# Performance work log

Measured on AMD Instinct MI355X. Metric: run time of the kernel, lower is better.

Reference implementation:

```python
import jax, jax.numpy as jnp
import numpy as np

BATCH, B_BANDS, C, T = 32, 5, 64, 128
D_EMBED, D_S = 64, 16


def setup_inputs() -> dict:
    key = jax.random.key(0)
    ks = jax.random.split(key, 8)
    x = jax.random.normal(ks[0], (BATCH, B_BANDS, C, T), dtype=jnp.float32)
    # sparse binary physical adjacency with self-loops (avoid all-masked rows)
    adj = (jax.random.uniform(ks[1], (C, C)) < 0.3).astype(jnp.float32)
    adj = adj.at[jnp.arange(C), jnp.arange(C)].set(1.0)
    active_mask = jnp.ones((BATCH, T, B_BANDS), dtype=jnp.float32)
    alpha = jax.random.uniform(ks[2], (BATCH, T, B_BANDS), dtype=jnp.float32) + 0.1
    active_alpha = alpha / alpha.sum(axis=-1, keepdims=True)
    # per-band Linear(1, d_embed): weight (d_embed,1) flattened to (d_embed,), bias (d_embed,)
    W_e = jax.random.normal(ks[3], (B_BANDS, D_EMBED), dtype=jnp.float32)  # kaiming-ish for fan_in=1
    b_e = jax.random.uniform(ks[4], (B_BANDS, D_EMBED), dtype=jnp.float32) * 2.0 - 1.0
    Wq = jax.random.normal(ks[5], (D_S, D_EMBED), dtype=jnp.float32) / np.sqrt(D_EMBED)
    Wk = jax.random.normal(ks[6], (D_S, D_EMBED), dtype=jnp.float32) / np.sqrt(D_EMBED)
    return {"x": x, "adj": adj, "active_mask": active_mask, "active_alpha": active_alpha,
            "W_e": W_e, "b_e": b_e, "Wq": Wq, "Wk": Wk}


def reference(x, adj, active_mask, active_alpha, W_e, b_e, Wq, Wk):
    # x: (batch, B, C, T) -> x_t: (batch, T, B, C)
    x_t = jnp.transpose(x, (0, 3, 1, 2))
    d_s = Wq.shape[0]
    # per-band Linear(1, d_embed), all bands vectorized: e (batch, T, B, C, d_embed)
    e = x_t[..., None] * W_e[None, None, :, None, :] + b_e[None, None, :, None, :]
    q = jnp.einsum('btncd,sd->btncs', e, Wq)
    k = jnp.einsum('btncd,sd->btncs', e, Wk)
    # scores per band: (batch, T, B, C, C)
    s = jnp.einsum('btnis,btnjs->btnij', q, k) / jnp.sqrt(jnp.asarray(d_s, x.dtype))
    neg_inf = jnp.finfo(s.dtype).min
    s = jnp.where(adj[None, None, None, :, :] > 0, s, neg_inf)
    P = jax.nn.softmax(s, axis=-1)  # row-stochastic on adj neighborhoods
    w = active_alpha * active_mask  # (batch, T, B)
    P_func = jnp.einsum('btn,btnij->btij', w, P)  # (batch, T, C, C)
    e_mean = e.mean(axis=3)  # (batch, T, B, d_embed) mean over electrodes
    embed_accum = jnp.einsum('btn,btnd->btd', active_mask, e_mean)
    active_count = jnp.clip(active_mask.sum(axis=-1, keepdims=True), 1.0, None)
    embeddings_mean = embed_accum / active_count
    return P_func, embeddings_mean
```

## Files before the change

kernel.cpp:

```cpp
#include <hip/hip_runtime.h>
#include <math.h>

#define NBANDS 5
#define T_TILE 4
#define PFUNC_ELEMS (32*128*64*64)
#define LOG2E 1.4426950408889634f

#define DPP_ADD(x, ctrl) \
    ((x) + __int_as_float(__builtin_amdgcn_update_dpp(0, __float_as_int(x), (ctrl), 0xF, 0xF, true)))

__global__ __launch_bounds__(512) void bfp_kernel(
        const float* __restrict__ x,
        const float* __restrict__ adj,
        const float* __restrict__ amask,
        const float* __restrict__ alpha,
        const float* __restrict__ We,
        const float* __restrict__ be,
        const float* __restrict__ Wq,
        const float* __restrict__ Wk,
        float* __restrict__ out) {
    const int bid = blockIdx.x;
    const int blk = (bid & 7) * 128 + (bid >> 3);
    const int bt0 = blk * T_TILE;
    const int b = bt0 >> 7;
    const int t0 = bt0 & 127;
    const int tid = threadIdx.x;

    __shared__ __align__(16) float x_s[T_TILE][NBANDS][64];
    __shared__ float xbar_s[T_TILE][NBANDS], xmax_s[T_TILE][NBANDS], xmin_s[T_TILE][NBANDS];
    __shared__ float w_s[T_TILE][NBANDS], mask_s[T_TILE][NBANDS];
    __shared__ float acw_s[NBANDS], bcw_s[NBANDS];

    const int i = tid >> 3;
    const int j0 = (tid & 7) << 3;

    const float4 a0 = *(const float4*)(adj + i * 64 + j0);
    const float4 a1 = *(const float4*)(adj + i * 64 + j0 + 4);

    float4 xstage;
    if (tid < NBANDS * 64)
        xstage = *(const float4*)(x + ((size_t)b * 320 + tid) * 128 + t0);

    if (tid >= 512 - T_TILE * NBANDS) {
        const int idx = tid - (512 - T_TILE * NBANDS);
        const size_t base = ((size_t)b * 128 + t0) * NBANDS;
        const int t = idx / NBANDS, n = idx % NBANDS;
        float mk = amask[base + idx];
        mask_s[t][n] = mk;
        w_s[t][n] = alpha[base + idx] * mk;
    }

    {
        const int wvid = tid >> 6;
        const int lane = tid & 63;
        if (wvid < NBANDS) {
            const int n = wvid;
            const int s = lane >> 2;
            const int d0c = (lane & 3) * 16;
            float u = 0.f, v = 0.f, w = 0.f;
            #pragma unroll
            for (int dd = 0; dd < 16; ++dd) {
                int d = d0c + dd;
                float we = We[n * 64 + d], bb = be[n * 64 + d];
                float wq = Wq[s * 64 + d], wk = Wk[s * 64 + d];
                u = fmaf(wq, we, u);
                v = fmaf(wk, we, v);
                w = fmaf(wq, bb, w);
            }
            #pragma unroll
            for (int mk = 1; mk <= 2; mk <<= 1) {
                u += __shfl_xor(u, mk);
                v += __shfl_xor(v, mk);
                w += __shfl_xor(w, mk);
            }
            float ac = u * v, bc = w * v;
            #pragma unroll
            for (int mk = 4; mk <= 32; mk <<= 1) {
                ac += __shfl_xor(ac, mk);
                bc += __shfl_xor(bc, mk);
            }
            if (lane == 0) {
                acw_s[n] = 0.25f * LOG2E * ac;
                bcw_s[n] = 0.25f * LOG2E * bc;
            }
        }
    }

    if (tid < NBANDS * 64) {
        const int n = tid >> 6, c = tid & 63;
        x_s[0][n][c] = xstage.x;
        x_s[1][n][c] = xstage.y;
        x_s[2][n][c] = xstage.z;
        x_s[3][n][c] = xstage.w;
    }
    __syncthreads();

    {
        const int wv = tid >> 6, lane = tid & 63;
        for (int pair = wv; pair < T_TILE * NBANDS; pair += 8) {
            const int t = pair & 3, n = pair >> 2;
            float v = x_s[t][n][lane];
            float sm = v, mx = v, mn = v;
            #pragma unroll
            for (int mk = 32; mk >= 1; mk >>= 1) {
                sm += __shfl_xor(sm, mk);
                mx = fmaxf(mx, __shfl_xor(mx, mk));
                mn = fminf(mn, __shfl_xor(mn, mk));
            }
            if (lane == 0) {
                xbar_s[t][n] = sm * (1.f / 64.f);
                xmax_s[t][n] = mx;
                xmin_s[t][n] = mn;
            }
        }
    }
    __syncthreads();

    if (tid < T_TILE * 64) {
        const int t = tid >> 6, d = tid & 63;
        float cnt = 0.f, accm = 0.f;
        #pragma unroll
        for (int n = 0; n < NBANDS; ++n) {
            cnt += mask_s[t][n];
            accm += mask_s[t][n] * fmaf(xbar_s[t][n], We[n * 64 + d], be[n * 64 + d]);
        }
        out[PFUNC_ELEMS + (size_t)(bt0 + t) * 64 + d] = accm / fmaxf(cnt, 1.f);
    }

    for (int t = 0; t < T_TILE; ++t) {
        float4 xv0[NBANDS], xv1[NBANDS];
        float gi[NBANDS];
        #pragma unroll
        for (int n = 0; n < NBANDS; ++n) {
            xv0[n] = ((const float4*)(&x_s[t][n][j0]))[0];
            xv1[n] = ((const float4*)(&x_s[t][n][j0]))[1];
            gi[n]  = x_s[t][n][i];
        }

        float acc[8];
        #pragma unroll
        for (int jj = 0; jj < 8; ++jj) acc[jj] = 0.f;

        #pragma unroll
        for (int n = 0; n < NBANDS; ++n) {
            const float g2 = fmaf(acw_s[n], gi[n], bcw_s[n]);
            const float negm = -fmaxf(g2 * xmax_s[t][n], g2 * xmin_s[t][n]);
            float e0 = __builtin_amdgcn_exp2f(fmaf(g2, xv0[n].x, negm));
            float e1 = __builtin_amdgcn_exp2f(fmaf(g2, xv0[n].y, negm));
            float e2 = __builtin_amdgcn_exp2f(fmaf(g2, xv0[n].z, negm));
            float e3 = __builtin_amdgcn_exp2f(fmaf(g2, xv0[n].w, negm));
            float e4 = __builtin_amdgcn_exp2f(fmaf(g2, xv1[n].x, negm));
            float e5 = __builtin_amdgcn_exp2f(fmaf(g2, xv1[n].y, negm));
            float e6 = __builtin_amdgcn_exp2f(fmaf(g2, xv1[n].z, negm));
            float e7 = __builtin_amdgcn_exp2f(fmaf(g2, xv1[n].w, negm));
            float z0 = e0 * a0.x;
            z0 = fmaf(e1, a0.y, z0);
            z0 = fmaf(e2, a0.z, z0);
            z0 = fmaf(e3, a0.w, z0);
            float z1 = e4 * a1.x;
            z1 = fmaf(e5, a1.y, z1);
            z1 = fmaf(e6, a1.z, z1);
            z1 = fmaf(e7, a1.w, z1);
            float Z = z0 + z1;
            Z = DPP_ADD(Z, 0xB1);
            Z = DPP_ADD(Z, 0x4E);
            Z = DPP_ADD(Z, 0x141);
            const float sc = w_s[t][n] * __builtin_amdgcn_rcpf(fmaxf(Z, 1e-30f));
            acc[0] = fmaf(e0, sc, acc[0]);
            acc[1] = fmaf(e1, sc, acc[1]);
            acc[2] = fmaf(e2, sc, acc[2]);
            acc[3] = fmaf(e3, sc, acc[3]);
            acc[4] = fmaf(e4, sc, acc[4]);
            acc[5] = fmaf(e5, sc, acc[5]);
            acc[6] = fmaf(e6, sc, acc[6]);
            acc[7] = fmaf(e7, sc, acc[7]);
        }

        float4* outp = (float4*)(out + ((size_t)(bt0 + t) * 64 + i) * 64 + j0);
        outp[0] = make_float4(acc[0] * a0.x, acc[1] * a0.y, acc[2] * a0.z, acc[3] * a0.w);
        outp[1] = make_float4(acc[4] * a1.x, acc[5] * a1.y, acc[6] * a1.z, acc[7] * a1.w);
    }
}

extern "C" void kernel_launch(void* const* d_in, const int* in_sizes, int n_in,
                              void* d_out, int out_size, void* d_ws, size_t ws_size,
                              hipStream_t stream) {
    const float* x     = (const float*)d_in[0];
    const float* adj   = (const float*)d_in[1];
    const float* amask = (const float*)d_in[2];
    const float* alpha = (const float*)d_in[3];
    const float* We    = (const float*)d_in[4];
    const float* be    = (const float*)d_in[5];
    const float* Wq    = (const float*)d_in[6];
    const float* Wk    = (const float*)d_in[7];
    float* out = (float*)d_out;

    bfp_kernel<<<1024, 512, 0, stream>>>(x, adj, amask, alpha, We, be, Wq, Wk, out);
}
```

Baseline: 30.95 us.

## Split into prep kernel for transpose/stats and per-timestep main kernel

Adds a prep kernel that transposes x into a workspace (b,t,n,c) layout and precomputes per-(b,t,n) max/min/mean, masked alpha and the band coefficients once. The main kernel then processes one timestep per block (4096 blocks) and reads these precomputed values instead of redoing reductions and coefficient dot products in every block. This removes redundant per-block setup and syncs, and gives more, smaller blocks. The cost is a second launch and an extra round trip through global memory for x. The old fused kernel stays as a fallback for when the workspace is too small.

```diff
diff --git a/kernel.cpp b/kernel.cpp
--- a/kernel.cpp
+++ b/kernel.cpp
@@ -2,82 +2,217 @@
 #include <math.h>
 
 #define NBANDS 5
-#define T_TILE 4
 #define PFUNC_ELEMS (32*128*64*64)
 #define LOG2E 1.4426950408889634f
 
+#define WS_XT    0
+#define WS_STATS 1310720
+#define WS_MASK  1392640
+#define WS_COEF  1413120
+#define WS_FLOATS_NEEDED 1413136ull
+
 #define DPP_ADD(x, ctrl) \
     ((x) + __int_as_float(__builtin_amdgcn_update_dpp(0, __float_as_int(x), (ctrl), 0xF, 0xF, true)))
 
-__global__ __launch_bounds__(512) void bfp_kernel(
+__global__ __launch_bounds__(256) void bfp_prep_kernel(
         const float* __restrict__ x,
-        const float* __restrict__ adj,
         const float* __restrict__ amask,
         const float* __restrict__ alpha,
-        const float* __restrict__ We,
-        const float* __restrict__ be,
-        const float* __restrict__ Wq,
-        const float* __restrict__ Wk,
+        const float* __restrict__ We, const float* __restrict__ be,
+        const float* __restrict__ Wq, const float* __restrict__ Wk,
+        float* __restrict__ ws) {
+    const int bid = blockIdx.x;
+    const int b = bid / NBANDS, n = bid % NBANDS;
+    const int tid = threadIdx.x;
+    __shared__ float xt[64][129];
+
+    for (int idx = tid; idx < 64 * 32; idx += 256) {
+        const int c = idx >> 5, q = idx & 31;
+        float4 v = *(const float4*)(x + (((size_t)b * NBANDS + n) * 64 + c) * 128 + q * 4);
+        xt[c][q * 4 + 0] = v.x;
+        xt[c][q * 4 + 1] = v.y;
+        xt[c][q * 4 + 2] = v.z;
+        xt[c][q * 4 + 3] = v.w;
+    }
+    __syncthreads();
+
+    for (int idx = tid; idx < 128 * 16; idx += 256) {
+        const int t = idx >> 4, cq = idx & 15;
+        float4 v = make_float4(xt[cq * 4 + 0][t], xt[cq * 4 + 1][t],
+                               xt[cq * 4 + 2][t], xt[cq * 4 + 3][t]);
+        *(float4*)(ws + WS_XT + (((size_t)b * 128 + t) * NBANDS + n) * 64 + cq * 4) = v;
+    }
+
+    if (tid < 128) {
+        const int t = tid;
+        float mx = xt[0][t], mn = mx, sm = mx;
+        #pragma unroll 8
+        for (int c = 1; c < 64; ++c) {
+            float v = xt[c][t];
+            mx = fmaxf(mx, v);
+            mn = fminf(mn, v);
+            sm += v;
+        }
+        const size_t sidx = ((size_t)b * 128 + t) * NBANDS + n;
+        const float am = amask[sidx];
+        ((float4*)(ws + WS_STATS))[sidx] =
+            make_float4(mx, mn, alpha[sidx] * am, sm * (1.f / 64.f));
+        ws[WS_MASK + sidx] = am;
+    }
+
+    if (b == 0 && tid < 16) {
+        const int s = tid;
+        float u = 0.f, v = 0.f, w = 0.f;
+        for (int d = 0; d < 64; ++d) {
+            const float we = We[n * 64 + d], bb = be[n * 64 + d];
+            u = fmaf(Wq[s * 64 + d], we, u);
+            v = fmaf(Wk[s * 64 + d], we, v);
+            w = fmaf(Wq[s * 64 + d], bb, w);
+        }
+        float ac = u * v, bc = w * v;
+        #pragma unroll
+        for (int mk = 1; mk <= 8; mk <<= 1) {
+            ac += __shfl_xor(ac, mk);
+            bc += __shfl_xor(bc, mk);
+        }
+        if (s == 0) {
+            ws[WS_COEF + n]     = 0.25f * LOG2E * ac;
+            ws[WS_COEF + 8 + n] = 0.25f * LOG2E * bc;
+        }
+    }
+}
+
+__global__ __launch_bounds__(512) void bfp_main_kernel(
+        const float* __restrict__ adj,
+        const float* __restrict__ We, const float* __restrict__ be,
+        const float* __restrict__ ws,
+        float* __restrict__ out) {
+    const int bid = blockIdx.x;
+    const int bt = (bid & 7) * 512 + (bid >> 3);
+    const int tid = threadIdx.x;
+    const int i = tid >> 3;
+    const int j0 = (tid & 7) << 3;
+
+    const float* xtp = ws + WS_XT + (size_t)bt * 320;
+    const float4* stp = (const float4*)(ws + WS_STATS) + (size_t)bt * NBANDS;
+
+    const float4 a0 = *(const float4*)(adj + i * 64 + j0);
+    const float4 a1 = *(const float4*)(adj + i * 64 + j0 + 4);
+
+    if (tid < 64) {
+        float cnt = 0.f, accm = 0.f;
+        #pragma unroll
+        for (int n = 0; n < NBANDS; ++n) {
+            const float mk = ws[WS_MASK + (size_t)bt * NBANDS + n];
+            cnt += mk;
+            accm += mk * fmaf(stp[n].w, We[n * 64 + tid], be[n * 64 + tid]);
+        }
+        out[PFUNC_ELEMS + (size_t)bt * 64 + tid] = accm / fmaxf(cnt, 1.f);
+    }
+
+    float acc[8];
+    #pragma unroll
+    for (int jj = 0; jj < 8; ++jj) acc[jj] = 0.f;
+
+    #pragma unroll
+    for (int n = 0; n < NBANDS; ++n) {
+        const float4 st = stp[n];
+        const float gi = xtp[n * 64 + i];
+        const float4 xv0 = *(const float4*)(xtp + n * 64 + j0);
+        const float4 xv1 = *(const float4*)(xtp + n * 64 + j0 + 4);
+        const float g2 = fmaf(ws[WS_COEF + n], gi, ws[WS_COEF + 8 + n]);
+        const float negm = -fmaxf(g2 * st.x, g2 * st.y);
+        float e0 = __builtin_amdgcn_exp2f(fmaf(g2, xv0.x, negm));
+        float e1 = __builtin_amdgcn_exp2f(fmaf(g2, xv0.y, negm));
+        float e2 = __builtin_amdgcn_exp2f(fmaf(g2, xv0.z, negm));
+        float e3 = __builtin_amdgcn_exp2f(fmaf(g2, xv0.w, negm));
+        float e4 = __builtin_amdgcn_exp2f(fmaf(g2, xv1.x, negm));
+        float e5 = __builtin_amdgcn_exp2f(fmaf(g2, xv1.y, negm));
+        float e6 = __builtin_amdgcn_exp2f(fmaf(g2, xv1.z, negm));
+        float e7 = __builtin_amdgcn_exp2f(fmaf(g2, xv1.w, negm));
+        float z0 = e0 * a0.x;
+        z0 = fmaf(e1, a0.y, z0);
+        z0 = fmaf(e2, a0.z, z0);
+        z0 = fmaf(e3, a0.w, z0);
+        float z1 = e4 * a1.x;
+        z1 = fmaf(e5, a1.y, z1);
+        z1 = fmaf(e6, a1.z, z1);
+        z1 = fmaf(e7, a1.w, z1);
+        float Z = z0 + z1;
+        Z = DPP_ADD(Z, 0xB1);
+        Z = DPP_ADD(Z, 0x4E);
+        Z = DPP_ADD(Z, 0x141);
+        const float sc = st.z * __builtin_amdgcn_rcpf(fmaxf(Z, 1e-30f));
+        acc[0] = fmaf(e0, sc, acc[0]);
+        acc[1] = fmaf(e1, sc, acc[1]);
+        acc[2] = fmaf(e2, sc, acc[2]);
+        acc[3] = fmaf(e3, sc, acc[3]);
+        acc[4] = fmaf(e4, sc, acc[4]);
+        acc[5] = fmaf(e5, sc, acc[5]);
+        acc[6] = fmaf(e6, sc, acc[6]);
+        acc[7] = fmaf(e7, sc, acc[7]);
+    }
+
+    float4* outp = (float4*)(out + ((size_t)bt * 64 + i) * 64 + j0);
+    outp[0] = make_float4(acc[0] * a0.x, acc[1] * a0.y, acc[2] * a0.z, acc[3] * a0.w);
+    outp[1] = make_float4(acc[4] * a1.x, acc[5] * a1.y, acc[6] * a1.z, acc[7] * a1.w);
+}
+
+__global__ __launch_bounds__(512) void bfp_fallback_kernel(
+        const float* __restrict__ x, const float* __restrict__ adj,
+        const float* __restrict__ amask, const float* __restrict__ alpha,
+        const float* __restrict__ We, const float* __restrict__ be,
+        const float* __restrict__ Wq, const float* __restrict__ Wk,
         float* __restrict__ out) {
     const int bid = blockIdx.x;
     const int blk = (bid & 7) * 128 + (bid >> 3);
-    const int bt0 = blk * T_TILE;
+    const int bt0 = blk * 4;
     const int b = bt0 >> 7;
     const int t0 = bt0 & 127;
     const int tid = threadIdx.x;
 
-    __shared__ __align__(16) float x_s[T_TILE][NBANDS][64];
-    __shared__ float xbar_s[T_TILE][NBANDS], xmax_s[T_TILE][NBANDS], xmin_s[T_TILE][NBANDS];
-    __shared__ float w_s[T_TILE][NBANDS], mask_s[T_TILE][NBANDS];
+    __shared__ __align__(16) float x_s[4][NBANDS][64];
+    __shared__ float xbar_s[4][NBANDS], xmax_s[4][NBANDS], xmin_s[4][NBANDS];
+    __shared__ float w_s[4][NBANDS], mask_s[4][NBANDS];
     __shared__ float acw_s[NBANDS], bcw_s[NBANDS];
 
     const int i = tid >> 3;
     const int j0 = (tid & 7) << 3;
-
     const float4 a0 = *(const float4*)(adj + i * 64 + j0);
     const float4 a1 = *(const float4*)(adj + i * 64 + j0 + 4);
 
     float4 xstage;
     if (tid < NBANDS * 64)
         xstage = *(const float4*)(x + ((size_t)b * 320 + tid) * 128 + t0);
-
-    if (tid >= 512 - T_TILE * NBANDS) {
-        const int idx = tid - (512 - T_TILE * NBANDS);
+    if (tid >= 512 - 4 * NBANDS) {
+        const int idx = tid - (512 - 4 * NBANDS);
         const size_t base = ((size_t)b * 128 + t0) * NBANDS;
         const int t = idx / NBANDS, n = idx % NBANDS;
         float mk = amask[base + idx];
         mask_s[t][n] = mk;
         w_s[t][n] = alpha[base + idx] * mk;
     }
-
     {
-        const int wvid = tid >> 6;
-        const int lane = tid & 63;
+        const int wvid = tid >> 6, lane = tid & 63;
         if (wvid < NBANDS) {
-            const int n = wvid;
-            const int s = lane >> 2;
-            const int d0c = (lane & 3) * 16;
+            const int n = wvid, s = lane >> 2, d0c = (lane & 3) * 16;
             float u = 0.f, v = 0.f, w = 0.f;
             #pragma unroll
             for (int dd = 0; dd < 16; ++dd) {
                 int d = d0c + dd;
                 float we = We[n * 64 + d], bb = be[n * 64 + d];
-                float wq = Wq[s * 64 + d], wk = Wk[s * 64 + d];
-                u = fmaf(wq, we, u);
-                v = fmaf(wk, we, v);
-                w = fmaf(wq, bb, w);
+                u = fmaf(Wq[s * 64 + d], we, u);
+                v = fmaf(Wk[s * 64 + d], we, v);
+                w = fmaf(Wq[s * 64 + d], bb, w);
             }
             #pragma unroll
             for (int mk = 1; mk <= 2; mk <<= 1) {
-                u += __shfl_xor(u, mk);
-                v += __shfl_xor(v, mk);
-                w += __shfl_xor(w, mk);
+                u += __shfl_xor(u, mk); v += __shfl_xor(v, mk); w += __shfl_xor(w, mk);
             }
             float ac = u * v, bc = w * v;
             #pragma unroll
             for (int mk = 4; mk <= 32; mk <<= 1) {
-                ac += __shfl_xor(ac, mk);
-                bc += __shfl_xor(bc, mk);
+                ac += __shfl_xor(ac, mk); bc += __shfl_xor(bc, mk);
             }
             if (lane == 0) {
                 acw_s[n] = 0.25f * LOG2E * ac;
@@ -85,19 +220,15 @@
             }
         }
     }
-
     if (tid < NBANDS * 64) {
         const int n = tid >> 6, c = tid & 63;
-        x_s[0][n][c] = xstage.x;
-        x_s[1][n][c] = xstage.y;
-        x_s[2][n][c] = xstage.z;
-        x_s[3][n][c] = xstage.w;
+        x_s[0][n][c] = xstage.x; x_s[1][n][c] = xstage.y;
+        x_s[2][n][c] = xstage.z; x_s[3][n][c] = xstage.w;
     }
     __syncthreads();
-
     {
         const int wv = tid >> 6, lane = tid & 63;
-        for (int pair = wv; pair < T_TILE * NBANDS; pair += 8) {
+        for (int pair = wv; pair < 4 * NBANDS; pair += 8) {
             const int t = pair & 3, n = pair >> 2;
             float v = x_s[t][n][lane];
             float sm = v, mx = v, mn = v;
@@ -109,14 +240,12 @@
             }
             if (lane == 0) {
                 xbar_s[t][n] = sm * (1.f / 64.f);
-                xmax_s[t][n] = mx;
-                xmin_s[t][n] = mn;
+                xmax_s[t][n] = mx; xmin_s[t][n] = mn;
             }
         }
     }
     __syncthreads();
-
-    if (tid < T_TILE * 64) {
+    if (tid < 4 * 64) {
         const int t = tid >> 6, d = tid & 63;
         float cnt = 0.f, accm = 0.f;
         #pragma unroll
@@ -126,21 +255,18 @@
         }
         out[PFUNC_ELEMS + (size_t)(bt0 + t) * 64 + d] = accm / fmaxf(cnt, 1.f);
     }
-
-    for (int t = 0; t < T_TILE; ++t) {
+    for (int t = 0; t < 4; ++t) {
         float4 xv0[NBANDS], xv1[NBANDS];
         float gi[NBANDS];
         #pragma unroll
         for (int n = 0; n < NBANDS; ++n) {
             xv0[n] = ((const float4*)(&x_s[t][n][j0]))[0];
             xv1[n] = ((const float4*)(&x_s[t][n][j0]))[1];
-            gi[n]  = x_s[t][n][i];
-        }
-
+            gi[n] = x_s[t][n][i];
+        }
         float acc[8];
         #pragma unroll
         for (int jj = 0; jj < 8; ++jj) acc[jj] = 0.f;
-
         #pragma unroll
         for (int n = 0; n < NBANDS; ++n) {
             const float g2 = fmaf(acw_s[n], gi[n], bcw_s[n]);
@@ -154,28 +280,17 @@
             float e6 = __builtin_amdgcn_exp2f(fmaf(g2, xv1[n].z, negm));
             float e7 = __builtin_amdgcn_exp2f(fmaf(g2, xv1[n].w, negm));
             float z0 = e0 * a0.x;
-            z0 = fmaf(e1, a0.y, z0);
-            z0 = fmaf(e2, a0.z, z0);
-            z0 = fmaf(e3, a0.w, z0);
+            z0 = fmaf(e1, a0.y, z0); z0 = fmaf(e2, a0.z, z0); z0 = fmaf(e3, a0.w, z0);
             float z1 = e4 * a1.x;
-            z1 = fmaf(e5, a1.y, z1);
-            z1 = fmaf(e6, a1.z, z1);
-            z1 = fmaf(e7, a1.w, z1);
+            z1 = fmaf(e5, a1.y, z1); z1 = fmaf(e6, a1.z, z1); z1 = fmaf(e7, a1.w, z1);
             float Z = z0 + z1;
-            Z = DPP_ADD(Z, 0xB1);
-            Z = DPP_ADD(Z, 0x4E);
-            Z = DPP_ADD(Z, 0x141);
+            Z = DPP_ADD(Z, 0xB1); Z = DPP_ADD(Z, 0x4E); Z = DPP_ADD(Z, 0x141);
             const float sc = w_s[t][n] * __builtin_amdgcn_rcpf(fmaxf(Z, 1e-30f));
-            acc[0] = fmaf(e0, sc, acc[0]);
-            acc[1] = fmaf(e1, sc, acc[1]);
-            acc[2] = fmaf(e2, sc, acc[2]);
-            acc[3] = fmaf(e3, sc, acc[3]);
-            acc[4] = fmaf(e4, sc, acc[4]);
-            acc[5] = fmaf(e5, sc, acc[5]);
-            acc[6] = fmaf(e6, sc, acc[6]);
-            acc[7] = fmaf(e7, sc, acc[7]);
-        }
-
+            acc[0] = fmaf(e0, sc, acc[0]); acc[1] = fmaf(e1, sc, acc[1]);
+            acc[2] = fmaf(e2, sc, acc[2]); acc[3] = fmaf(e3, sc, acc[3]);
+            acc[4] = fmaf(e4, sc, acc[4]); acc[5] = fmaf(e5, sc, acc[5]);
+            acc[6] = fmaf(e6, sc, acc[6]); acc[7] = fmaf(e7, sc, acc[7]);
+        }
         float4* outp = (float4*)(out + ((size_t)(bt0 + t) * 64 + i) * 64 + j0);
         outp[0] = make_float4(acc[0] * a0.x, acc[1] * a0.y, acc[2] * a0.z, acc[3] * a0.w);
         outp[1] = make_float4(acc[4] * a1.x, acc[5] * a1.y, acc[6] * a1.z, acc[7] * a1.w);
@@ -193,7 +308,13 @@
     const float* be    = (const float*)d_in[5];
     const float* Wq    = (const float*)d_in[6];
     const float* Wk    = (const float*)d_in[7];
+    float* ws  = (float*)d_ws;
     float* out = (float*)d_out;
 
-    bfp_kernel<<<1024, 512, 0, stream>>>(x, adj, amask, alpha, We, be, Wq, Wk, out);
+    if (ws_size >= WS_FLOATS_NEEDED * sizeof(float)) {
+        bfp_prep_kernel<<<160, 256, 0, stream>>>(x, amask, alpha, We, be, Wq, Wk, ws);
+        bfp_main_kernel<<<4096, 512, 0, stream>>>(adj, We, be, ws, out);
+    } else {
+        bfp_fallback_kernel<<<1024, 512, 0, stream>>>(x, adj, amask, alpha, We, be, Wq, Wk, out);
+    }
 }
```

Measured after the change: 34.26 us. 1.11x slower.
